# Kernel tuning notes

Measured on AMD Instinct MI355X. Metric: run time of the kernel, lower is better.

The kernel has to match this reference:

```python
import jax, jax.numpy as jnp
import numpy as np

B, FIN, H, W = 16, 256, 32, 32
NH, FH = 8, 64
CIN = FIN + 2  # fin + 2 coordinate-grid pos channels
COUT = NH * FH


def setup_inputs() -> dict:
    key = jax.random.key(0)
    ks = jax.random.split(key, 9)
    s = 1.0 / np.sqrt(CIN)
    so = 1.0 / np.sqrt(COUT)
    return {
        "x": jax.random.normal(ks[0], (B, FIN, H, W), dtype=jnp.float32),
        "wq": jax.random.uniform(ks[1], (COUT, CIN), jnp.float32, -s, s),
        "bq": jax.random.uniform(ks[2], (COUT,), jnp.float32, -s, s),
        "wk": jax.random.uniform(ks[3], (COUT, CIN), jnp.float32, -s, s),
        "bk": jax.random.uniform(ks[4], (COUT,), jnp.float32, -s, s),
        "wv": jax.random.uniform(ks[5], (COUT, CIN), jnp.float32, -s, s),
        "bv": jax.random.uniform(ks[6], (COUT,), jnp.float32, -s, s),
        "wo": jax.random.uniform(ks[7], (FIN, COUT), jnp.float32, -so, so),
        "bo": jax.random.uniform(ks[8], (FIN,), jnp.float32, -so, so),
    }


def reference(x, wq, bq, wk, bk, wv, bv, wo, bo):
    b, c, h, w = x.shape
    n = h * w
    # PosEncoding: concat one linspace(-1,1) coordinate channel per spatial dim
    gy, gx = jnp.meshgrid(jnp.linspace(-1.0, 1.0, h), jnp.linspace(-1.0, 1.0, w), indexing="ij")
    pos = jnp.broadcast_to(jnp.stack([gy, gx])[None], (b, 2, h, w)).astype(x.dtype)
    t = jnp.concatenate([x, pos], axis=1).reshape(b, c + 2, n)  # [B, C+2, N]
    # 1x1 convs are per-token GEMMs
    q = (jnp.einsum("oc,bcn->bon", wq, t) + bq[:, None]).reshape(b, NH, FH, n)
    k = (jnp.einsum("oc,bcn->bon", wk, t) + bk[:, None]).reshape(b, NH, FH, n)
    v = (jnp.einsum("oc,bcn->bon", wv, t) + bv[:, None]).reshape(b, NH, FH, n)
    temp = FH ** 0.5
    attn = jax.nn.softmax(jnp.einsum("bhdn,bhdm->bhnm", q, k) / temp, axis=-1)
    o = jnp.einsum("bhnm,bhdm->bhdn", attn, v).reshape(b, NH * FH, n)
    o = jnp.einsum("oc,bcn->bon", wo, o) + bo[:, None]
    return x + o.reshape(b, c, h, w)
```

## Files before the change

### kernel.cpp

```cpp
#include <hip/hip_runtime.h>


typedef unsigned short u16;
typedef unsigned int   u32;
typedef __attribute__((ext_vector_type(8))) short  short8;
typedef __attribute__((ext_vector_type(4))) float  float4_;

#define MFMA16(a, b, c) __builtin_amdgcn_mfma_f32_16x16x32_bf16(a, b, c, 0, 0, 0)

__device__ __forceinline__ float bf2f(u16 u) {
    union { u32 i; float f; } v; v.i = ((u32)u) << 16; return v.f;
}
__device__ __forceinline__ u16 f2bf(float f) {
    union { float f; u32 i; } v; v.f = f;
    u32 r = v.i + 0x7FFFu + ((v.i >> 16) & 1u);
    return (u16)(r >> 16);
}
__device__ __forceinline__ u16 f2bf_fast(float f) {
    union { float f; u32 i; } v; v.f = f;
    return (u16)((v.i + 0x8000u) >> 16);
}

__global__ __launch_bounds__(256) void prep(
    const float* __restrict__ wq, const float* __restrict__ wk,
    const float* __restrict__ wv, const float* __restrict__ x,
    u16* __restrict__ wb, u16* __restrict__ xT)
{
    __shared__ float Lt[64][65];
    const int bid = blockIdx.x;
    const int tid = threadIdx.x;
    if (bid < 512) {
        int i = bid * 256 + tid;
        int o = i >> 8, c = i & 255;
        size_t si = (size_t)o * 258 + c;
        wb[i]          = f2bf(wq[si]);
        wb[131072 + i] = f2bf(wk[si]);
        wb[262144 + i] = f2bf(wv[si]);
    } else {
        int r = bid - 512;
        int n0 = (r & 15) * 64, c0 = ((r >> 4) & 3) * 64, b = r >> 6;
#pragma unroll
        for (int p = 0; p < 4; ++p) {
            int c = p * 16 + (tid >> 4);
            int nn = (tid & 15) * 4;
            float4 v = *(const float4*)&x[((size_t)(b * 256) + c0 + c) * 1024 + n0 + nn];
            Lt[c][nn + 0] = v.x; Lt[c][nn + 1] = v.y;
            Lt[c][nn + 2] = v.z; Lt[c][nn + 3] = v.w;
        }
        __syncthreads();
#pragma unroll
        for (int p = 0; p < 4; ++p) {
            int n = p * 16 + (tid >> 4);
            int cc = (tid & 15) * 4;
            ushort4 st;
            st.x = f2bf(Lt[cc + 0][n]); st.y = f2bf(Lt[cc + 1][n]);
            st.z = f2bf(Lt[cc + 2][n]); st.w = f2bf(Lt[cc + 3][n]);
            *(ushort4*)&xT[((size_t)(b << 10) + n0 + n) * 256 + c0 + cc] = st;
        }
    }
}

__global__ __launch_bounds__(256) void qkv_mfma(
    const u16* __restrict__ xT, const u16* __restrict__ wb,
    const float* __restrict__ wq, const float* __restrict__ wk,
    const float* __restrict__ wv,
    const float* __restrict__ bq, const float* __restrict__ bk,
    const float* __restrict__ bv,
    u16* __restrict__ qkvbuf)
{
    __shared__ u16 Wl[128][40];
    __shared__ u16 Tl[128][40];
    const int tid = threadIdx.x;
    const int lane = tid & 63, w = tid >> 6;
    const int quad = lane >> 4, m15 = lane & 15;
    const int n0 = blockIdx.x * 128, mt = blockIdx.y, b = blockIdx.z;
    const int mat = mt >> 2;
    const int m0 = mt * 128;
    const float* worig = (mat == 0) ? wq : ((mat == 1) ? wk : wv);
    const float* bias  = (mat == 0) ? bq : ((mat == 1) ? bk : bv);
    const float oscale = (mat == 1) ? 0.125f : 1.0f;
    u16* outbuf = qkvbuf + (size_t)mat * 8388608;

    float4_ acc[2][8];
#pragma unroll
    for (int s = 0; s < 2; ++s)
#pragma unroll
        for (int t = 0; t < 8; ++t) acc[s][t] = (float4_){0, 0, 0, 0};

    const int row = tid >> 2, col8 = (tid & 3) * 8;

    for (int cc0 = 0; cc0 < 256; cc0 += 32) {
        __syncthreads();
#pragma unroll
        for (int rr = 0; rr < 128; rr += 64) {
            *(short8*)&Wl[row + rr][col8] =
                *(const short8*)(wb + (size_t)(m0 + row + rr) * 256 + cc0 + col8);
            *(short8*)&Tl[row + rr][col8] =
                *(const short8*)(xT + ((size_t)(b << 10) + n0 + row + rr) * 256 + cc0 + col8);
        }
        __syncthreads();
        short8 af[2];
#pragma unroll
        for (int s = 0; s < 2; ++s)
            af[s] = *(const short8*)&Wl[w * 32 + s * 16 + m15][quad * 8];
#pragma unroll
        for (int t = 0; t < 8; ++t) {
            short8 bf = *(const short8*)&Tl[t * 16 + m15][quad * 8];
#pragma unroll
            for (int s = 0; s < 2; ++s)
                acc[s][t] = MFMA16(af[s], bf, acc[s][t]);
        }
    }

#pragma unroll
    for (int s = 0; s < 2; ++s) {
        float wg[4], wx[4], bi[4];
#pragma unroll
        for (int r = 0; r < 4; ++r) {
            int om = (mt & 3) * 128 + w * 32 + s * 16 + quad * 4 + r;
            wg[r] = worig[(size_t)om * 258 + 256];
            wx[r] = worig[(size_t)om * 258 + 257];
            bi[r] = bias[om];
        }
        const int h = (mt & 3) * 2 + ((w * 32 + s * 16) >> 6);
        const int dbase = ((w * 32 + s * 16) & 63) + quad * 4;
#pragma unroll
        for (int t = 0; t < 8; ++t) {
            int n = n0 + t * 16 + m15;
            float gy = -1.0f + 2.0f * (float)(n >> 5) / 31.0f;
            float gx = -1.0f + 2.0f * (float)(n & 31) / 31.0f;
            float v[4];
#pragma unroll
            for (int r = 0; r < 4; ++r)
                v[r] = (acc[s][t][r] + wg[r] * gy + wx[r] * gx + bi[r]) * oscale;
            if (mat != 2) {
                ushort4 st;
                st.x = f2bf(v[0]); st.y = f2bf(v[1]);
                st.z = f2bf(v[2]); st.w = f2bf(v[3]);
                *(ushort4*)&outbuf[((size_t)(b * 8 + h) * 1024 + n) * 64 + dbase] = st;
            } else {
#pragma unroll
                for (int r = 0; r < 4; ++r)
                    outbuf[((size_t)(b * 8 + h) * 64 + dbase + r) * 1024 + n] = f2bf(v[r]);
            }
        }
    }
}

__global__ __launch_bounds__(256) void attn_mfma(
    u16* __restrict__ qbuf, const u16* __restrict__ kbuf,
    const u16* __restrict__ vbuf)
{
    __shared__ u16 Kl[64][72];
    __shared__ u16 Vl[64][72];
    __shared__ u16 Pl[4][32][72];

    const int tid = threadIdx.x;
    const int lane = tid & 63, w = tid >> 6;
    const int quad = lane >> 4, m15 = lane & 15;
    const int q0 = blockIdx.x * 128;
    const int bh = blockIdx.y;
    u16* qb = qbuf + (size_t)bh * 65536;
    const u16* kb = kbuf + (size_t)bh * 65536;
    const u16* vb = vbuf + (size_t)bh * 65536;

    short8 qf[2][2];
#pragma unroll
    for (int s = 0; s < 2; ++s) {
        const u16* qr = qb + (size_t)(q0 + w * 32 + s * 16 + m15) * 64 + quad * 8;
        qf[s][0] = *(const short8*)qr;
        qf[s][1] = *(const short8*)(qr + 32);
    }

    float4_ O[2][4];
    float lp[2][4];
#pragma unroll
    for (int s = 0; s < 2; ++s)
#pragma unroll
        for (int t = 0; t < 4; ++t) { O[s][t] = (float4_){0,0,0,0}; lp[s][t] = 0.0f; }

    const int row = tid >> 3, c8 = (tid & 7) * 8;

    for (int kt0 = 0; kt0 < 1024; kt0 += 64) {
        __syncthreads();
#pragma unroll
        for (int rr = 0; rr < 64; rr += 32) {
            *(short8*)&Kl[row + rr][c8] =
                *(const short8*)(kb + (size_t)(kt0 + row + rr) * 64 + c8);
            *(short8*)&Vl[row + rr][c8] =
                *(const short8*)(vb + (size_t)(row + rr) * 1024 + kt0 + c8);
        }
        __syncthreads();

        float4_ S[2][4];
#pragma unroll
        for (int s = 0; s < 2; ++s)
#pragma unroll
            for (int t = 0; t < 4; ++t) S[s][t] = (float4_){0, 0, 0, 0};
#pragma unroll
        for (int c = 0; c < 2; ++c) {
            short8 bk[4];
#pragma unroll
            for (int t = 0; t < 4; ++t)
                bk[t] = *(const short8*)&Kl[t * 16 + m15][c * 32 + quad * 8];
#pragma unroll
            for (int s = 0; s < 2; ++s)
#pragma unroll
                for (int t = 0; t < 4; ++t)
                    S[s][t] = MFMA16(qf[s][c], bk[t], S[s][t]);
        }

#pragma unroll
        for (int s = 0; s < 2; ++s)
#pragma unroll
            for (int r = 0; r < 4; ++r) {
                float p0 = __expf(S[s][0][r]);
                float p1 = __expf(S[s][1][r]);
                float p2 = __expf(S[s][2][r]);
                float p3 = __expf(S[s][3][r]);
                u16* pr = &Pl[w][s * 16 + quad * 4 + r][m15];
                pr[0]  = f2bf_fast(p0);
                pr[16] = f2bf_fast(p1);
                pr[32] = f2bf_fast(p2);
                pr[48] = f2bf_fast(p3);
                lp[s][r] += (p0 + p1) + (p2 + p3);
            }

#pragma unroll
        for (int c = 0; c < 2; ++c) {
            short8 av[4];
#pragma unroll
            for (int dt = 0; dt < 4; ++dt)
                av[dt] = *(const short8*)&Vl[dt * 16 + m15][c * 32 + quad * 8];
#pragma unroll
            for (int s = 0; s < 2; ++s) {
                short8 bp = *(const short8*)&Pl[w][s * 16 + m15][c * 32 + quad * 8];
#pragma unroll
                for (int dt = 0; dt < 4; ++dt)
                    O[s][dt] = MFMA16(av[dt], bp, O[s][dt]);
            }
        }
    }

#pragma unroll
    for (int s = 0; s < 2; ++s)
#pragma unroll
        for (int r = 0; r < 4; ++r) {
            float v = lp[s][r];
            v += __shfl_xor(v, 1);
            v += __shfl_xor(v, 2);
            v += __shfl_xor(v, 4);
            v += __shfl_xor(v, 8);
            lp[s][r] = v;
        }

#pragma unroll
    for (int s = 0; s < 2; ++s) {
        int src = (m15 >> 2) * 16;
        float a0 = __shfl(lp[s][0], src);
        float a1 = __shfl(lp[s][1], src);
        float a2 = __shfl(lp[s][2], src);
        float a3 = __shfl(lp[s][3], src);
        int rr2 = m15 & 3;
        float lq = (rr2 & 2) ? ((rr2 & 1) ? a3 : a2) : ((rr2 & 1) ? a1 : a0);
        float linv = 1.0f / lq;
        int n = q0 + w * 32 + s * 16 + m15;
#pragma unroll
        for (int dt = 0; dt < 4; ++dt) {
            ushort4 st;
            st.x = f2bf(O[s][dt][0] * linv);
            st.y = f2bf(O[s][dt][1] * linv);
            st.z = f2bf(O[s][dt][2] * linv);
            st.w = f2bf(O[s][dt][3] * linv);
            *(ushort4*)&qb[(size_t)n * 64 + dt * 16 + quad * 4] = st;
        }
    }
}

__global__ __launch_bounds__(256) void proj_mfma(
    const u16* __restrict__ ao, const float* __restrict__ wo,
    const float* __restrict__ bo, const float* __restrict__ x,
    float* __restrict__ out)
{
    __shared__ u16 Wl[64][72];
    __shared__ u16 Tl[64][72];
    const int tid = threadIdx.x;
    const int lane = tid & 63, w = tid >> 6;
    const int quad = lane >> 4, m15 = lane & 15;
    const int n0 = blockIdx.x * 64, f0 = blockIdx.y * 64, b = blockIdx.z;

    float4_ acc[4] = {{0,0,0,0},{0,0,0,0},{0,0,0,0},{0,0,0,0}};
    const int row = tid >> 3, c8 = (tid & 7) * 8;

    for (int cc0 = 0; cc0 < 512; cc0 += 64) {
        __syncthreads();
        const int h = cc0 >> 6;
#pragma unroll
        for (int rr = 0; rr < 64; rr += 32) {
            const float* wsrc = wo + (size_t)(f0 + row + rr) * 512 + cc0 + c8;
            float4 v0 = *(const float4*)wsrc;
            float4 v1 = *(const float4*)(wsrc + 4);
            ushort4 s0, s1;
            s0.x = f2bf(v0.x); s0.y = f2bf(v0.y); s0.z = f2bf(v0.z); s0.w = f2bf(v0.w);
            s1.x = f2bf(v1.x); s1.y = f2bf(v1.y); s1.z = f2bf(v1.z); s1.w = f2bf(v1.w);
            *(ushort4*)&Wl[row + rr][c8]     = s0;
            *(ushort4*)&Wl[row + rr][c8 + 4] = s1;
            *(short8*)&Tl[row + rr][c8] =
                *(const short8*)(ao + ((size_t)((b << 3) + h) * 1024 + n0 + row + rr) * 64 + c8);
        }
        __syncthreads();
#pragma unroll
        for (int c = 0; c < 2; ++c) {
            short8 af = *(const short8*)&Wl[w * 16 + m15][c * 32 + quad * 8];
#pragma unroll
            for (int t = 0; t < 4; ++t) {
                short8 bf = *(const short8*)&Tl[t * 16 + m15][c * 32 + quad * 8];
                acc[t] = MFMA16(af, bf, acc[t]);
            }
        }
    }

    float bi[4];
#pragma unroll
    for (int r = 0; r < 4; ++r) bi[r] = bo[f0 + w * 16 + quad * 4 + r];
#pragma unroll
    for (int t = 0; t < 4; ++t) {
        int n = n0 + t * 16 + m15;
#pragma unroll
        for (int r = 0; r < 4; ++r) {
            int f = f0 + w * 16 + quad * 4 + r;
            size_t idx = ((size_t)(b * 256) + f) * 1024 + n;
            out[idx] = acc[t][r] + bi[r] + x[idx];
        }
    }
}

extern "C" void kernel_launch(void* const* d_in, const int* in_sizes, int n_in,
                              void* d_out, int out_size, void* d_ws, size_t ws_size,
                              hipStream_t stream) {
    const float* x  = (const float*)d_in[0];
    const float* wq = (const float*)d_in[1];
    const float* bq = (const float*)d_in[2];
    const float* wk = (const float*)d_in[3];
    const float* bk = (const float*)d_in[4];
    const float* wv = (const float*)d_in[5];
    const float* bv = (const float*)d_in[6];
    const float* wo = (const float*)d_in[7];
    const float* bo = (const float*)d_in[8];

    u16* qkvbuf = (u16*)d_ws;
    u16* region = qkvbuf + 3 * 8388608;
    u16* xT = region;
    u16* wb = region + 4194304;

    prep<<<1536, 256, 0, stream>>>(wq, wk, wv, x, wb, xT);

    qkv_mfma<<<dim3(8, 12, 16), 256, 0, stream>>>(
        xT, wb, wq, wk, wv, bq, bk, bv, qkvbuf);

    attn_mfma<<<dim3(8, 128), 256, 0, stream>>>(
        qkvbuf, qkvbuf + 8388608, qkvbuf + 16777216);

    proj_mfma<<<dim3(16, 4, 16), 256, 0, stream>>>(qkvbuf, wo, bo, x, (float*)d_out);
}
```

Baseline: 202.9 us.

## Prefetch next K/V tile into registers, swizzle P in LDS, add MFMA priority

```diff
diff --git a/kernel.cpp b/kernel.cpp
--- a/kernel.cpp
+++ b/kernel.cpp
@@ -147,7 +147,7 @@
     }
 }
 
-__global__ __launch_bounds__(256) void attn_mfma(
+__global__ __launch_bounds__(256, 4) void attn_mfma(
     u16* __restrict__ qbuf, const u16* __restrict__ kbuf,
     const u16* __restrict__ vbuf)
 {
@@ -180,17 +180,28 @@
         for (int t = 0; t < 4; ++t) { O[s][t] = (float4_){0,0,0,0}; lp[s][t] = 0.0f; }
 
     const int row = tid >> 3, c8 = (tid & 7) * 8;
+    const int psw = (quad & 2) * 8;
+    const int rsw = (m15 & 8) * 2;
+
+    short8 kr0 = *(const short8*)(kb + (size_t)row * 64 + c8);
+    short8 kr1 = *(const short8*)(kb + (size_t)(row + 32) * 64 + c8);
+    short8 vr0 = *(const short8*)(vb + (size_t)row * 1024 + c8);
+    short8 vr1 = *(const short8*)(vb + (size_t)(row + 32) * 1024 + c8);
+    *(short8*)&Kl[row][c8]      = kr0;
+    *(short8*)&Kl[row + 32][c8] = kr1;
+    *(short8*)&Vl[row][c8]      = vr0;
+    *(short8*)&Vl[row + 32][c8] = vr1;
+    __syncthreads();
 
     for (int kt0 = 0; kt0 < 1024; kt0 += 64) {
-        __syncthreads();
-#pragma unroll
-        for (int rr = 0; rr < 64; rr += 32) {
-            *(short8*)&Kl[row + rr][c8] =
-                *(const short8*)(kb + (size_t)(kt0 + row + rr) * 64 + c8);
-            *(short8*)&Vl[row + rr][c8] =
-                *(const short8*)(vb + (size_t)(row + rr) * 1024 + kt0 + c8);
-        }
-        __syncthreads();
+        const bool more = (kt0 < 960);
+        if (more) {
+            const int ktn = kt0 + 64;
+            kr0 = *(const short8*)(kb + (size_t)(ktn + row) * 64 + c8);
+            kr1 = *(const short8*)(kb + (size_t)(ktn + row + 32) * 64 + c8);
+            vr0 = *(const short8*)(vb + (size_t)row * 1024 + ktn + c8);
+            vr1 = *(const short8*)(vb + (size_t)(row + 32) * 1024 + ktn + c8);
+        }
 
         float4_ S[2][4];
 #pragma unroll
@@ -203,11 +214,13 @@
 #pragma unroll
             for (int t = 0; t < 4; ++t)
                 bk[t] = *(const short8*)&Kl[t * 16 + m15][c * 32 + quad * 8];
+            __builtin_amdgcn_s_setprio(1);
 #pragma unroll
             for (int s = 0; s < 2; ++s)
 #pragma unroll
                 for (int t = 0; t < 4; ++t)
                     S[s][t] = MFMA16(qf[s][c], bk[t], S[s][t]);
+            __builtin_amdgcn_s_setprio(0);
         }
 
 #pragma unroll
@@ -219,10 +232,10 @@
                 float p2 = __expf(S[s][2][r]);
                 float p3 = __expf(S[s][3][r]);
                 u16* pr = &Pl[w][s * 16 + quad * 4 + r][m15];
-                pr[0]  = f2bf_fast(p0);
-                pr[16] = f2bf_fast(p1);
-                pr[32] = f2bf_fast(p2);
-                pr[48] = f2bf_fast(p3);
+                pr[0 ^ psw]  = f2bf_fast(p0);
+                pr[16 ^ psw] = f2bf_fast(p1);
+                pr[32 ^ psw] = f2bf_fast(p2);
+                pr[48 ^ psw] = f2bf_fast(p3);
                 lp[s][r] += (p0 + p1) + (p2 + p3);
             }
 
@@ -234,11 +247,22 @@
                 av[dt] = *(const short8*)&Vl[dt * 16 + m15][c * 32 + quad * 8];
 #pragma unroll
             for (int s = 0; s < 2; ++s) {
-                short8 bp = *(const short8*)&Pl[w][s * 16 + m15][c * 32 + quad * 8];
+                short8 bp = *(const short8*)&Pl[w][s * 16 + m15][(c * 32 + quad * 8) ^ rsw];
+                __builtin_amdgcn_s_setprio(1);
 #pragma unroll
                 for (int dt = 0; dt < 4; ++dt)
                     O[s][dt] = MFMA16(av[dt], bp, O[s][dt]);
+                __builtin_amdgcn_s_setprio(0);
             }
+        }
+
+        __syncthreads();
+        if (more) {
+            *(short8*)&Kl[row][c8]      = kr0;
+            *(short8*)&Kl[row + 32][c8] = kr1;
+            *(short8*)&Vl[row][c8]      = vr0;
+            *(short8*)&Vl[row + 32][c8] = vr1;
+            __syncthreads();
         }
     }
 
```

Result: slower. 221.1 us (+9.0%).

## Double-buffer K/V tiles via direct global-to-LDS loads with XOR swizzle

Applied to the files above, without the earlier changes.

```diff
diff --git a/kernel.cpp b/kernel.cpp
--- a/kernel.cpp
+++ b/kernel.cpp
@@ -7,6 +7,9 @@
 typedef __attribute__((ext_vector_type(4))) float  float4_;
 
 #define MFMA16(a, b, c) __builtin_amdgcn_mfma_f32_16x16x32_bf16(a, b, c, 0, 0, 0)
+#define GLOAD_LDS16(g, l) \
+    __builtin_amdgcn_global_load_lds((const __attribute__((address_space(1))) void*)(g), \
+                                     (__attribute__((address_space(3))) void*)(l), 16, 0, 0)
 
 __device__ __forceinline__ float bf2f(u16 u) {
     union { u32 i; float f; } v; v.i = ((u32)u) << 16; return v.f;
@@ -151,8 +154,8 @@
     u16* __restrict__ qbuf, const u16* __restrict__ kbuf,
     const u16* __restrict__ vbuf)
 {
-    __shared__ u16 Kl[64][72];
-    __shared__ u16 Vl[64][72];
+    __shared__ __align__(1024) u16 Ksh[2][4096];
+    __shared__ __align__(1024) u16 Vsh[2][4096];
     __shared__ u16 Pl[4][32][72];
 
     const int tid = threadIdx.x;
@@ -164,6 +167,9 @@
     const u16* kb = kbuf + (size_t)bh * 65536;
     const u16* vb = vbuf + (size_t)bh * 65536;
 
+    const int lr = lane >> 3, li = lane & 7;
+    const int swoff = (li * 16) ^ (lr << 4);
+
     short8 qf[2][2];
 #pragma unroll
     for (int s = 0; s < 2; ++s) {
@@ -179,18 +185,33 @@
 #pragma unroll
         for (int t = 0; t < 4; ++t) { O[s][t] = (float4_){0,0,0,0}; lp[s][t] = 0.0f; }
 
-    const int row = tid >> 3, c8 = (tid & 7) * 8;
-
+#pragma unroll
+    for (int i = 0; i < 2; ++i) {
+        const int ch = w * 2 + i;
+        const int grow = ch * 8 + lr;
+        GLOAD_LDS16((const char*)kb + (size_t)grow * 128 + swoff,
+                    &Ksh[0][ch * 512]);
+        GLOAD_LDS16((const char*)vb + (size_t)grow * 2048 + swoff,
+                    &Vsh[0][ch * 512]);
+    }
+    __syncthreads();
+
+    int cur = 0;
     for (int kt0 = 0; kt0 < 1024; kt0 += 64) {
-        __syncthreads();
-#pragma unroll
-        for (int rr = 0; rr < 64; rr += 32) {
-            *(short8*)&Kl[row + rr][c8] =
-                *(const short8*)(kb + (size_t)(kt0 + row + rr) * 64 + c8);
-            *(short8*)&Vl[row + rr][c8] =
-                *(const short8*)(vb + (size_t)(row + rr) * 1024 + kt0 + c8);
-        }
-        __syncthreads();
+        if (kt0 < 960) {
+            const int ktn = kt0 + 64;
+#pragma unroll
+            for (int i = 0; i < 2; ++i) {
+                const int ch = w * 2 + i;
+                const int grow = ch * 8 + lr;
+                GLOAD_LDS16((const char*)kb + (size_t)(ktn + grow) * 128 + swoff,
+                            &Ksh[cur ^ 1][ch * 512]);
+                GLOAD_LDS16((const char*)vb + (size_t)grow * 2048 + ktn * 2 + swoff,
+                            &Vsh[cur ^ 1][ch * 512]);
+            }
+        }
+        const u16* Kc = &Ksh[cur][0];
+        const u16* Vc = &Vsh[cur][0];
 
         float4_ S[2][4];
 #pragma unroll
@@ -202,12 +223,15 @@
             short8 bk[4];
 #pragma unroll
             for (int t = 0; t < 4; ++t)
-                bk[t] = *(const short8*)&Kl[t * 16 + m15][c * 32 + quad * 8];
+                bk[t] = *(const short8*)&Kc[(t * 16 + m15) * 64 +
+                                            ((c * 32 + quad * 8) ^ ((m15 & 7) << 3))];
+            __builtin_amdgcn_s_setprio(1);
 #pragma unroll
             for (int s = 0; s < 2; ++s)
 #pragma unroll
                 for (int t = 0; t < 4; ++t)
                     S[s][t] = MFMA16(qf[s][c], bk[t], S[s][t]);
+            __builtin_amdgcn_s_setprio(0);
         }
 
 #pragma unroll
@@ -231,15 +255,21 @@
             short8 av[4];
 #pragma unroll
             for (int dt = 0; dt < 4; ++dt)
-                av[dt] = *(const short8*)&Vl[dt * 16 + m15][c * 32 + quad * 8];
+                av[dt] = *(const short8*)&Vc[(dt * 16 + m15) * 64 +
+                                             ((c * 32 + quad * 8) ^ ((m15 & 7) << 3))];
 #pragma unroll
             for (int s = 0; s < 2; ++s) {
                 short8 bp = *(const short8*)&Pl[w][s * 16 + m15][c * 32 + quad * 8];
+                __builtin_amdgcn_s_setprio(1);
 #pragma unroll
                 for (int dt = 0; dt < 4; ++dt)
                     O[s][dt] = MFMA16(av[dt], bp, O[s][dt]);
-            }
-        }
+                __builtin_amdgcn_s_setprio(0);
+            }
+        }
+
+        __syncthreads();
+        cur ^= 1;
     }
 
 #pragma unroll
```

Result: no change. 204.6 us (+0.8%).
